# Performance work log

Hardware: AMD Instinct MI355X
Metric: run time of the kernel (lower is better)

## Reference

```python
import jax, jax.numpy as jnp
import numpy as np
from itertools import permutations

NUM_SPEAKERS = 4
EPS = 1e-07


def setup_inputs() -> dict:
    key = jax.random.key(0)
    k1, k2 = jax.random.split(key)
    B, T, S = 128, 16384, NUM_SPEAKERS
    pred = jax.random.uniform(k1, (B, T, S), dtype=jnp.float32)
    target = jax.random.uniform(k2, (B, T, S), dtype=jnp.float32)
    mask = jnp.ones((B, T), dtype=jnp.float32)
    return {"pred": pred, "target": target, "mask": mask}


def reference(pred, target, mask):
    # pred, target: [B, T, S]; mask: [B, T]
    B, T, S = pred.shape
    p = jnp.clip(pred, EPS, 1.0 - EPS)
    logp = jnp.log(p)          # [B,T,S]
    log1mp = jnp.log1p(-p)     # [B,T,S]
    # Pairwise BCE: bce[b,t,i,j] = -(target[b,t,j]*log p[b,t,i] + (1-target[b,t,j])*log(1-p[b,t,i]))
    bce = -(target[:, :, None, :] * logp[:, :, :, None]
            + (1.0 - target[:, :, None, :]) * log1mp[:, :, :, None])  # [B,T,S,S]
    denom = jnp.sum(mask, axis=1)  # [B]
    # Masked mean over time, mean over prediction-speaker axis i -> cost matrix C[b,i,j]
    C = jnp.einsum('btij,bt->bij', bce, mask) / (S * denom)[:, None, None]  # [B,S,S]
    perms = jnp.asarray(list(permutations(range(S))), dtype=jnp.int32)  # [P,S]
    # perm_losses[b,p] = sum_i C[b, i, perms[p,i]] / S? no: mean over i already folded via /S above
    idx_i = jnp.arange(S)[None, :]            # [1,S]
    perm_losses = jnp.sum(C[:, idx_i, perms], axis=-1)  # [B,P]
    min_loss = jnp.min(perm_losses, axis=-1)  # [B]
    best_idx = jnp.argmin(perm_losses, axis=-1)  # [B] index into perms
    loss = jnp.mean(min_loss)
    best_perms = perms[best_idx]  # [B,S]
    return loss, best_perms
```

## Files before the change

### kernel.cpp

```cpp
#include <hip/hip_runtime.h>

#define TPB    256
#define CHUNKS 8
#define NACC   21
#define NPERM  24

__constant__ int c_perm[NPERM][4] = {
    {0,1,2,3},{0,1,3,2},{0,2,1,3},{0,2,3,1},{0,3,1,2},{0,3,2,1},
    {1,0,2,3},{1,0,3,2},{1,2,0,3},{1,2,3,0},{1,3,0,2},{1,3,2,0},
    {2,0,1,3},{2,0,3,1},{2,1,0,3},{2,1,3,0},{2,3,0,1},{2,3,1,0},
    {3,0,1,2},{3,0,2,1},{3,1,0,2},{3,1,2,0},{3,2,0,1},{3,2,1,0}
};

__global__ __launch_bounds__(TPB) void pit_partial(
    const float* __restrict__ pred, const float* __restrict__ target,
    const float* __restrict__ mask, float* __restrict__ partial, int T)
{
    const int b      = blockIdx.x / CHUNKS;
    const int chunk  = blockIdx.x - b * CHUNKS;
    const int tPerBlock = (T + CHUNKS - 1) / CHUNKS;
    const int tid    = threadIdx.x;
    const int base   = chunk * tPerBlock;
    const int tEnd   = min(base + tPerBlock, T);

    const float4* p4  = (const float4*)pred   + (size_t)b * T;
    const float4* t4  = (const float4*)target + (size_t)b * T;
    const float* mrow = mask + (size_t)b * T;

    float D[4][4] = {{0.f,0.f,0.f,0.f},{0.f,0.f,0.f,0.f},
                     {0.f,0.f,0.f,0.f},{0.f,0.f,0.f,0.f}};
    float S1[4] = {0.f,0.f,0.f,0.f};
    float dn = 0.f;

    const float lo = 1e-7f;
    const float hi = 1.0f - 1e-7f;

    for (int t = base + tid; t < tEnd; t += TPB) {
        float4 pv = p4[t];
        float4 tv = t4[t];
        float m   = mrow[t];
        float pp[4] = {pv.x, pv.y, pv.z, pv.w};
        float tt[4] = {tv.x, tv.y, tv.z, tv.w};
        float lp[4], lq[4];
        #pragma unroll
        for (int s = 0; s < 4; ++s) {
            float p = fminf(fmaxf(pp[s], lo), hi);
            lp[s] = __logf(p);
            lq[s] = __logf(1.0f - p);
        }
        dn += m;
        float mt[4];
        #pragma unroll
        for (int j = 0; j < 4; ++j) mt[j] = m * tt[j];
        #pragma unroll
        for (int i = 0; i < 4; ++i) {
            S1[i] = fmaf(m, lq[i], S1[i]);
            float d = lq[i] - lp[i];
            #pragma unroll
            for (int j = 0; j < 4; ++j) D[i][j] = fmaf(d, mt[j], D[i][j]);
        }
    }

    float acc[NACC];
    #pragma unroll
    for (int i = 0; i < 4; ++i)
        #pragma unroll
        for (int j = 0; j < 4; ++j) acc[i * 4 + j] = D[i][j];
    #pragma unroll
    for (int i = 0; i < 4; ++i) acc[16 + i] = S1[i];
    acc[20] = dn;

    #pragma unroll
    for (int k = 0; k < NACC; ++k) {
        float v = acc[k];
        #pragma unroll
        for (int off = 32; off > 0; off >>= 1)
            v += __shfl_xor(v, off, 64);
        acc[k] = v;
    }

    __shared__ float sred[TPB / 64][NACC];
    const int wave = tid >> 6;
    const int lane = tid & 63;
    if (lane == 0) {
        #pragma unroll
        for (int k = 0; k < NACC; ++k) sred[wave][k] = acc[k];
    }
    __syncthreads();
    if (tid < NACC) {
        float v = 0.f;
        #pragma unroll
        for (int w = 0; w < TPB / 64; ++w) v += sred[w][tid];
        partial[(size_t)blockIdx.x * NACC + tid] = v;
    }
}

__global__ __launch_bounds__(128) void pit_final(
    const float* __restrict__ partial, float* __restrict__ out, int B)
{
    const int b = threadIdx.x;
    float minv = 0.f;

    if (b < B) {
        float A[NACC];
        #pragma unroll
        for (int k = 0; k < NACC; ++k) A[k] = 0.f;
        for (int c = 0; c < CHUNKS; ++c) {
            const float* src = partial + (size_t)(b * CHUNKS + c) * NACC;
            #pragma unroll
            for (int k = 0; k < NACC; ++k) A[k] += src[k];
        }
        const float inv = 1.0f / (4.0f * A[20]);
        float C[4][4];
        #pragma unroll
        for (int i = 0; i < 4; ++i)
            #pragma unroll
            for (int j = 0; j < 4; ++j)
                C[i][j] = (A[i * 4 + j] - A[16 + i]) * inv;

        minv = 3.4e38f;
        int mini = 0;
        #pragma unroll
        for (int p = 0; p < NPERM; ++p) {
            float v = C[0][c_perm[p][0]] + C[1][c_perm[p][1]]
                    + C[2][c_perm[p][2]] + C[3][c_perm[p][3]];
            if (v < minv) { minv = v; mini = p; }
        }
        #pragma unroll
        for (int i = 0; i < 4; ++i)
            out[1 + b * 4 + i] = (float)c_perm[mini][i];
    }

    float v = minv;
    #pragma unroll
    for (int off = 32; off > 0; off >>= 1)
        v += __shfl_xor(v, off, 64);
    __shared__ float ssum[16];
    const int wave = threadIdx.x >> 6;
    const int nwaves = blockDim.x >> 6;
    if ((threadIdx.x & 63) == 0) ssum[wave] = v;
    __syncthreads();
    if (threadIdx.x == 0) {
        float s = 0.f;
        for (int w = 0; w < nwaves; ++w) s += ssum[w];
        out[0] = s / (float)B;
    }
}

extern "C" void kernel_launch(void* const* d_in, const int* in_sizes, int n_in,
                              void* d_out, int out_size, void* d_ws, size_t ws_size,
                              hipStream_t stream)
{
    const float* pred   = (const float*)d_in[0];
    const float* target = (const float*)d_in[1];
    const float* mask   = (const float*)d_in[2];
    float* out     = (float*)d_out;
    float* partial = (float*)d_ws;

    const int B = (out_size - 1) / 4;
    const int T = in_sizes[2] / B;

    pit_partial<<<B * CHUNKS, TPB, 0, stream>>>(pred, target, mask, partial, T);
    pit_final<<<1, 128, 0, stream>>>(partial, out, B);
}
```

Baseline: 109.9 us.

## Fuse partial and final kernels via last-block ticket; unroll loads by four

Merges the two-kernel reduction into one kernel: each block writes its partial sums, then takes a ticket with an atomic counter, and the last block to finish does the permutation search and the final mean. The main loop is unrolled four-wide so each thread issues several independent loads before computing. This removes the second kernel launch and raises memory-level parallelism. In exchange it adds a memset launch for the counter, and the tail work is serialized in a single block.

```diff
diff --git a/kernel.cpp b/kernel.cpp
--- a/kernel.cpp
+++ b/kernel.cpp
@@ -12,9 +12,38 @@
     {3,0,1,2},{3,0,2,1},{3,1,0,2},{3,1,2,0},{3,2,0,1},{3,2,1,0}
 };
 
-__global__ __launch_bounds__(TPB) void pit_partial(
+__device__ __forceinline__ void accum_row(const float4 pv, const float4 tv, const float m,
+                                          float (&D)[4][4], float (&S1)[4], float& dn)
+{
+    const float lo = 1e-7f;
+    const float hi = 1.0f - 1e-7f;
+    float pp[4] = {pv.x, pv.y, pv.z, pv.w};
+    float tt[4] = {tv.x, tv.y, tv.z, tv.w};
+    float lp[4], lq[4];
+    #pragma unroll
+    for (int s = 0; s < 4; ++s) {
+        float p = fminf(fmaxf(pp[s], lo), hi);
+        lp[s] = __logf(p);
+        lq[s] = __logf(1.0f - p);
+    }
+    dn += m;
+    float mt[4];
+    #pragma unroll
+    for (int j = 0; j < 4; ++j) mt[j] = m * tt[j];
+    #pragma unroll
+    for (int i = 0; i < 4; ++i) {
+        S1[i] = fmaf(m, lq[i], S1[i]);
+        float d = lq[i] - lp[i];
+        #pragma unroll
+        for (int j = 0; j < 4; ++j) D[i][j] = fmaf(d, mt[j], D[i][j]);
+    }
+}
+
+__global__ __launch_bounds__(TPB, 4) void pit_fused(
     const float* __restrict__ pred, const float* __restrict__ target,
-    const float* __restrict__ mask, float* __restrict__ partial, int T)
+    const float* __restrict__ mask, float* __restrict__ partial,
+    unsigned int* __restrict__ ticket, float* __restrict__ out,
+    int T, int B)
 {
     const int b      = blockIdx.x / CHUNKS;
     const int chunk  = blockIdx.x - b * CHUNKS;
@@ -32,34 +61,22 @@
     float S1[4] = {0.f,0.f,0.f,0.f};
     float dn = 0.f;
 
-    const float lo = 1e-7f;
-    const float hi = 1.0f - 1e-7f;
-
-    for (int t = base + tid; t < tEnd; t += TPB) {
-        float4 pv = p4[t];
-        float4 tv = t4[t];
-        float m   = mrow[t];
-        float pp[4] = {pv.x, pv.y, pv.z, pv.w};
-        float tt[4] = {tv.x, tv.y, tv.z, tv.w};
-        float lp[4], lq[4];
+    int t0 = base + tid;
+    for (; t0 + 3 * TPB < tEnd; t0 += 4 * TPB) {
+        float4 pv[4], tv[4];
+        float  mv[4];
         #pragma unroll
-        for (int s = 0; s < 4; ++s) {
-            float p = fminf(fmaxf(pp[s], lo), hi);
-            lp[s] = __logf(p);
-            lq[s] = __logf(1.0f - p);
-        }
-        dn += m;
-        float mt[4];
+        for (int r = 0; r < 4; ++r) pv[r] = p4[t0 + r * TPB];
         #pragma unroll
-        for (int j = 0; j < 4; ++j) mt[j] = m * tt[j];
+        for (int r = 0; r < 4; ++r) tv[r] = t4[t0 + r * TPB];
         #pragma unroll
-        for (int i = 0; i < 4; ++i) {
-            S1[i] = fmaf(m, lq[i], S1[i]);
-            float d = lq[i] - lp[i];
-            #pragma unroll
-            for (int j = 0; j < 4; ++j) D[i][j] = fmaf(d, mt[j], D[i][j]);
-        }
+        for (int r = 0; r < 4; ++r) mv[r] = mrow[t0 + r * TPB];
+        #pragma unroll
+        for (int r = 0; r < 4; ++r)
+            accum_row(pv[r], tv[r], mv[r], D, S1, dn);
     }
+    for (; t0 < tEnd; t0 += TPB)
+        accum_row(p4[t0], t4[t0], mrow[t0], D, S1, dn);
 
     float acc[NACC];
     #pragma unroll
@@ -80,6 +97,7 @@
     }
 
     __shared__ float sred[TPB / 64][NACC];
+    __shared__ unsigned int s_last;
     const int wave = tid >> 6;
     const int lane = tid & 63;
     if (lane == 0) {
@@ -87,26 +105,30 @@
         for (int k = 0; k < NACC; ++k) sred[wave][k] = acc[k];
     }
     __syncthreads();
-    if (tid < NACC) {
-        float v = 0.f;
+
+    if (tid == 0) {
         #pragma unroll
-        for (int w = 0; w < TPB / 64; ++w) v += sred[w][tid];
-        partial[(size_t)blockIdx.x * NACC + tid] = v;
+        for (int k = 0; k < NACC; ++k) {
+            float v = sred[0][k] + sred[1][k] + sred[2][k] + sred[3][k];
+            partial[(size_t)blockIdx.x * NACC + k] = v;
+        }
+        __threadfence();
+        unsigned int old = atomicAdd(ticket, 1u);
+        s_last = (old == (unsigned int)(gridDim.x - 1)) ? 1u : 0u;
     }
-}
+    __syncthreads();
+    if (s_last == 0u) return;
 
-__global__ __launch_bounds__(128) void pit_final(
-    const float* __restrict__ partial, float* __restrict__ out, int B)
-{
-    const int b = threadIdx.x;
-    float minv = 0.f;
+    __threadfence();
 
-    if (b < B) {
+    float sumMin = 0.f;
+    for (int bb = tid; bb < B; bb += TPB) {
         float A[NACC];
         #pragma unroll
         for (int k = 0; k < NACC; ++k) A[k] = 0.f;
+        #pragma unroll
         for (int c = 0; c < CHUNKS; ++c) {
-            const float* src = partial + (size_t)(b * CHUNKS + c) * NACC;
+            const float* src = partial + (size_t)(bb * CHUNKS + c) * NACC;
             #pragma unroll
             for (int k = 0; k < NACC; ++k) A[k] += src[k];
         }
@@ -118,7 +140,7 @@
             for (int j = 0; j < 4; ++j)
                 C[i][j] = (A[i * 4 + j] - A[16 + i]) * inv;
 
-        minv = 3.4e38f;
+        float minv = 3.4e38f;
         int mini = 0;
         #pragma unroll
         for (int p = 0; p < NPERM; ++p) {
@@ -128,21 +150,21 @@
         }
         #pragma unroll
         for (int i = 0; i < 4; ++i)
-            out[1 + b * 4 + i] = (float)c_perm[mini][i];
+            out[1 + bb * 4 + i] = (float)c_perm[mini][i];
+        sumMin += minv;
     }
 
-    float v = minv;
+    float v = sumMin;
     #pragma unroll
     for (int off = 32; off > 0; off >>= 1)
         v += __shfl_xor(v, off, 64);
-    __shared__ float ssum[16];
-    const int wave = threadIdx.x >> 6;
-    const int nwaves = blockDim.x >> 6;
-    if ((threadIdx.x & 63) == 0) ssum[wave] = v;
+    __shared__ float ssum[TPB / 64];
+    if (lane == 0) ssum[wave] = v;
     __syncthreads();
-    if (threadIdx.x == 0) {
+    if (tid == 0) {
         float s = 0.f;
-        for (int w = 0; w < nwaves; ++w) s += ssum[w];
+        #pragma unroll
+        for (int w = 0; w < TPB / 64; ++w) s += ssum[w];
         out[0] = s / (float)B;
     }
 }
@@ -154,12 +176,14 @@
     const float* pred   = (const float*)d_in[0];
     const float* target = (const float*)d_in[1];
     const float* mask   = (const float*)d_in[2];
-    float* out     = (float*)d_out;
-    float* partial = (float*)d_ws;
+    float* out = (float*)d_out;
+
+    unsigned int* ticket = (unsigned int*)d_ws;
+    float* partial = (float*)((char*)d_ws + 256);
 
     const int B = (out_size - 1) / 4;
     const int T = in_sizes[2] / B;
 
-    pit_partial<<<B * CHUNKS, TPB, 0, stream>>>(pred, target, mask, partial, T);
-    pit_final<<<1, 128, 0, stream>>>(partial, out, B);
+    hipMemsetAsync(d_ws, 0, sizeof(unsigned int), stream);
+    pit_fused<<<B * CHUNKS, TPB, 0, stream>>>(pred, target, mask, partial, ticket, out, T, B);
 }
```

New measurement: 139.9 us. 27.3% more time.
